# Kernel optimization log

Hardware: AMD Instinct MI355X
Metric: run time of the kernel (lower is better)

The kernel has to match this reference:

```python
import jax, jax.numpy as jnp
import numpy as np

D_MODEL = 1024
NUM_HEADS = 16
HEAD_DIM = D_MODEL // NUM_HEADS
B, T = 4, 2048


def setup_inputs() -> dict:
    key = jax.random.key(0)
    ks = jax.random.split(key, 6)
    s = 1.0 / np.sqrt(D_MODEL)  # ~ nn.Linear init scale
    return {
        "x_q": jax.random.normal(ks[0], (B, T, D_MODEL), jnp.float32),
        "x_kv": jax.random.normal(ks[1], (B, T, D_MODEL), jnp.float32),
        "Wq": jax.random.uniform(ks[2], (D_MODEL, D_MODEL), jnp.float32, -s, s),
        "Wk": jax.random.uniform(ks[3], (D_MODEL, D_MODEL), jnp.float32, -s, s),
        "Wv": jax.random.uniform(ks[4], (D_MODEL, D_MODEL), jnp.float32, -s, s),
        "Wo": jax.random.uniform(ks[5], (D_MODEL, D_MODEL), jnp.float32, -s, s),
    }


def reference(x_q, x_kv, Wq, Wk, Wv, Wo):
    Bq, Tq, C = x_q.shape
    Tk = x_kv.shape[1]
    # torch nn.Linear: y = x @ W.T
    q = (x_q @ Wq.T).reshape(Bq, Tq, NUM_HEADS, HEAD_DIM).transpose(0, 2, 1, 3)
    k = (x_kv @ Wk.T).reshape(Bq, Tk, NUM_HEADS, HEAD_DIM).transpose(0, 2, 1, 3)
    v = (x_kv @ Wv.T).reshape(Bq, Tk, NUM_HEADS, HEAD_DIM).transpose(0, 2, 1, 3)
    scores = jnp.einsum("bhqd,bhkd->bhqk", q, k) / jnp.sqrt(
        jnp.asarray(HEAD_DIM, x_q.dtype)
    )
    causal = jnp.triu(jnp.ones((Tq, Tk), bool), k=1)  # True above diagonal
    scores = jnp.where(causal, -jnp.inf, scores)
    attn = jax.nn.softmax(scores, axis=-1)
    out = jnp.einsum("bhqk,bhkd->bhqd", attn, v)
    out = out.transpose(0, 2, 1, 3).reshape(Bq, Tq, C)
    return out @ Wo.T
```

## Files before the change

### kernel.cpp

```cpp
#include <hip/hip_runtime.h>
#include <stdint.h>

#define T_SEQ 2048
#define NH 16
#define HD 64
#define DM 1024
#define BB 4
#define MROWS (BB * T_SEQ)

#define QSCALE 0.18033688011112042f

typedef __attribute__((ext_vector_type(8))) __bf16 bf16x8;
typedef __attribute__((ext_vector_type(8))) unsigned short u16x8;
typedef __attribute__((ext_vector_type(4))) unsigned short u16x4;
typedef __attribute__((ext_vector_type(4))) float f32x4;

__device__ __forceinline__ unsigned short f2bf(float f) {
  return __builtin_bit_cast(unsigned short, (__bf16)f);
}

__device__ __forceinline__ bf16x8 ld8_f32(const float* __restrict__ p) {
  f32x4 a = *(const f32x4*)p;
  f32x4 b = *(const f32x4*)(p + 4);
  u16x8 u;
#pragma unroll
  for (int i = 0; i < 4; ++i) {
    u[i]     = f2bf(a[i]);
    u[i + 4] = f2bf(b[i]);
  }
  return __builtin_bit_cast(bf16x8, u);
}

__device__ __forceinline__ bf16x8 ld8_bf(const unsigned short* p) {
  return __builtin_bit_cast(bf16x8, *(const u16x8*)p);
}

__device__ __forceinline__ bf16x8 ld8_lds(const unsigned short* p) {
  u16x4 a = *(const u16x4*)p;
  u16x4 b = *(const u16x4*)(p + 4);
  return __builtin_bit_cast(bf16x8,
      __builtin_shufflevector(a, b, 0, 1, 2, 3, 4, 5, 6, 7));
}

__device__ __forceinline__ u16x4 lo4(u16x8 v) {
  return __builtin_shufflevector(v, v, 0, 1, 2, 3);
}
__device__ __forceinline__ u16x4 hi4(u16x8 v) {
  return __builtin_shufflevector(v, v, 4, 5, 6, 7);
}

__device__ __forceinline__ void gload_lds16(const unsigned short* g,
                                            unsigned short* l) {
  __builtin_amdgcn_global_load_lds(
      (const __attribute__((address_space(1))) unsigned int*)g,
      (__attribute__((address_space(3))) unsigned int*)l, 16, 0, 0);
}

__global__ __launch_bounds__(256) void conv_stage1(
    const float* __restrict__ Wk, const float* __restrict__ Wv,
    const float* __restrict__ Wq, const float* __restrict__ Wo,
    const float* __restrict__ xkv, const float* __restrict__ xq,
    unsigned short* __restrict__ Wkb012, unsigned short* __restrict__ Wob,
    unsigned short* __restrict__ Sxkv, unsigned short* __restrict__ Sxq) {
  const int bid = blockIdx.x;
  const int WSEG = (DM * DM / 8) / 256;
  const int XSEG = (MROWS * DM / 8) / 256;
  if (bid < 4 * WSEG) {
    const int w = bid >> 9;
    const float* src = (w == 0) ? Wk : (w == 1) ? Wv : (w == 2) ? Wq : Wo;
    unsigned short* dst = (w < 3) ? Wkb012 + (size_t)w * DM * DM : Wob;
    const int i = (bid & (WSEG - 1)) * 256 + threadIdx.x;
    *(u16x8*)(dst + (size_t)i * 8) =
        __builtin_bit_cast(u16x8, ld8_f32(src + (size_t)i * 8));
  } else if (bid < 4 * WSEG + XSEG) {
    const int i = (bid - 4 * WSEG) * 256 + threadIdx.x;
    *(u16x8*)(Sxkv + (size_t)i * 8) =
        __builtin_bit_cast(u16x8, ld8_f32(xkv + (size_t)i * 8));
  } else {
    const int i = (bid - 4 * WSEG - XSEG) * 256 + threadIdx.x;
    *(u16x8*)(Sxq + (size_t)i * 8) =
        __builtin_bit_cast(u16x8, ld8_f32(xq + (size_t)i * 8));
  }
}

template <int MODE>
__global__ __launch_bounds__(256) void gemm128(
    const unsigned short* __restrict__ A, const unsigned short* __restrict__ A2,
    const unsigned short* __restrict__ B, void* __restrict__ Cv,
    void* __restrict__ Cv2, void* __restrict__ Cv3, int M, int N, int K) {
  __shared__ __align__(16) unsigned short As[2][2][128 * 32];
  __shared__ __align__(16) unsigned short Bs[2][2][128 * 32];

  const int t = threadIdx.x;
  const int lane = t & 63, wave = t >> 6;
  const int lin = (int)(blockIdx.x + gridDim.x * blockIdx.y);
  const int nx = N >> 7;
  const int mpx = (M >> 7) >> 3;
  const int xcd = lin & 7, slot = lin >> 3;
  const int m0 = (xcd * mpx + slot / nx) * 128;
  const int n0 = (slot % nx) * 128;

  const unsigned short* Ause = A;
  if constexpr (MODE == 5) {
    if (n0 >= 2 * DM) Ause = A2;
  }

  const int srow = t >> 2;
  const int scol = (t & 3) * 8;
  const unsigned short* ga0 = Ause + (size_t)(m0 + srow) * K + scol;
  const unsigned short* ga1 = Ause + (size_t)(m0 + 64 + srow) * K + scol;
  const unsigned short* gb0 = B + (size_t)(n0 + srow) * K + scol;
  const unsigned short* gb1 = B + (size_t)(n0 + 64 + srow) * K + scol;
  const int lo0 = (wave * 16) * 32, lo1 = (64 + wave * 16) * 32;

  const int mw = (wave >> 1) * 64, nw = (wave & 1) * 64;
  const int fr = lane & 15, fq = (lane >> 4) * 8;

  f32x4 acc[4][4];
#pragma unroll
  for (int i = 0; i < 4; ++i)
#pragma unroll
    for (int j = 0; j < 4; ++j) acc[i][j] = (f32x4){0.f, 0.f, 0.f, 0.f};

  auto stage = [&](int buf, int k0) {
    gload_lds16(ga0 + k0,      &As[buf][0][lo0]);
    gload_lds16(ga1 + k0,      &As[buf][0][lo1]);
    gload_lds16(gb0 + k0,      &Bs[buf][0][lo0]);
    gload_lds16(gb1 + k0,      &Bs[buf][0][lo1]);
    gload_lds16(ga0 + k0 + 32, &As[buf][1][lo0]);
    gload_lds16(ga1 + k0 + 32, &As[buf][1][lo1]);
    gload_lds16(gb0 + k0 + 32, &Bs[buf][1][lo0]);
    gload_lds16(gb1 + k0 + 32, &Bs[buf][1][lo1]);
  };

  stage(0, 0);
  __syncthreads();

  const int NT = K >> 6;
  int cur = 0;
  for (int kt = 0; kt < NT; ++kt) {
    if (kt + 1 < NT) stage(cur ^ 1, (kt + 1) << 6);
#pragma unroll
    for (int ks = 0; ks < 2; ++ks) {
      bf16x8 af[4], bfr[4];
#pragma unroll
      for (int i = 0; i < 4; ++i)
        af[i] = ld8_bf(&As[cur][ks][(mw + i * 16 + fr) * 32 + fq]);
#pragma unroll
      for (int j = 0; j < 4; ++j)
        bfr[j] = ld8_bf(&Bs[cur][ks][(nw + j * 16 + fr) * 32 + fq]);
#pragma unroll
      for (int i = 0; i < 4; ++i)
#pragma unroll
        for (int j = 0; j < 4; ++j)
          acc[i][j] = __builtin_amdgcn_mfma_f32_16x16x32_bf16(
              af[i], bfr[j], acc[i][j], 0, 0, 0);
    }
    __syncthreads();
    cur ^= 1;
  }

  const int orow = (lane >> 4) * 4, ocol = lane & 15;
#pragma unroll
  for (int i = 0; i < 4; ++i)
#pragma unroll
    for (int j = 0; j < 4; ++j) {
      const int mb = m0 + mw + i * 16 + orow;
      const int n = n0 + nw + j * 16 + ocol;
      if constexpr (MODE == 5) {
        if (n0 < DM) {
#pragma unroll
          for (int r = 0; r < 4; ++r)
            ((unsigned short*)Cv)[(size_t)(mb + r) * DM + n] =
                f2bf(acc[i][j][r]);
        } else if (n0 < 2 * DM) {
          const int nv = n - DM;
          u16x4 pk;
#pragma unroll
          for (int r = 0; r < 4; ++r) pk[r] = f2bf(acc[i][j][r]);
          unsigned short* dst = (unsigned short*)Cv2 +
              ((size_t)((mb >> 11) * NH + (nv >> 6)) * HD + (nv & 63)) *
                  T_SEQ +
              (mb & 2047);
          *(u16x4*)dst = pk;
        } else {
          const int nq = n - 2 * DM;
#pragma unroll
          for (int r = 0; r < 4; ++r)
            ((unsigned short*)Cv3)[(size_t)(mb + r) * DM + nq] =
                f2bf(acc[i][j][r] * QSCALE);
        }
      } else {
#pragma unroll
        for (int r = 0; r < 4; ++r)
          ((float*)Cv)[(size_t)(mb + r) * N + n] = acc[i][j][r];
      }
    }
}

#define ASTR 68

__global__ __launch_bounds__(256, 2) void attn_flash2(
    const unsigned short* Qw, const unsigned short* __restrict__ Kw,
    const unsigned short* __restrict__ Vt, unsigned short* Ow) {
  __shared__ __align__(16) unsigned short k_lds[2][64][ASTR];
  __shared__ __align__(16) unsigned short vt_lds[2][64][ASTR];
  __shared__ __align__(16) unsigned short p_lds[4][32][ASTR];

  const int tid = threadIdx.x, lane = tid & 63, wave = tid >> 6;
  const int c16 = lane & 15, quad = lane >> 4;
  const int b = blockIdx.z, h = blockIdx.y;
  const int pi = blockIdx.x;
  const int qb0A = (15 - pi) * 128;
  const int qb0B = pi * 128;
  const size_t rkbase = (size_t)b * T_SEQ * DM + (size_t)h * HD;
  const size_t vtbase = (size_t)(b * NH + h) * HD * T_SEQ;

  const int q_loA = qb0A + wave * 32;
  const int q_loB = qb0B + wave * 32;

  bf16x8 qfA[2][2], qfB[2][2];
#pragma unroll
  for (int nf = 0; nf < 2; ++nf) {
    const unsigned short* qpA =
        Qw + rkbase + (size_t)(q_loA + nf * 16 + c16) * DM + quad * 8;
    qfA[nf][0] = ld8_bf(qpA);
    qfA[nf][1] = ld8_bf(qpA + 32);
    const unsigned short* qpB =
        Qw + rkbase + (size_t)(q_loB + nf * 16 + c16) * DM + quad * 8;
    qfB[nf][0] = ld8_bf(qpB);
    qfB[nf][1] = ld8_bf(qpB + 32);
  }

  f32x4 oA[2][4], oB[2][4];
#pragma unroll
  for (int nf = 0; nf < 2; ++nf)
#pragma unroll
    for (int j = 0; j < 4; ++j) {
      oA[nf][j] = (f32x4){0.f, 0.f, 0.f, 0.f};
      oB[nf][j] = (f32x4){0.f, 0.f, 0.f, 0.f};
    }
  float mA[2] = {-3.0e38f, -3.0e38f}, lA[2] = {0.f, 0.f};
  float mB[2] = {-3.0e38f, -3.0e38f}, lB[2] = {0.f, 0.f};

  const int srow = tid >> 2;
  const int scol = (tid & 3) * 16;
  const int ntiles = (qb0A + 191) >> 6;
  const int ntA_w = (q_loA + 95) >> 6;
  const int ntB_w = (q_loB + 95) >> 6;

  const unsigned short* kp0 = Kw + rkbase + (size_t)srow * DM + scol;
  const unsigned short* vp0 = Vt + vtbase + (size_t)srow * T_SEQ + scol;

  auto subtile = [&](const bf16x8 (&qf)[2][2], f32x4 (&o)[2][4],
                     float (&m_r)[2], float (&l_r)[2], const int q_lo,
                     const int kb0, const int bi) {
    f32x4 s[4][2];
    __builtin_amdgcn_s_setprio(1);
#pragma unroll
    for (int mf = 0; mf < 4; ++mf) {
      const unsigned short* kr = &k_lds[bi][mf * 16 + c16][quad * 8];
      const bf16x8 k0 = ld8_lds(kr);
      const bf16x8 k1 = ld8_lds(kr + 32);
#pragma unroll
      for (int nf = 0; nf < 2; ++nf) {
        f32x4 a = {0.f, 0.f, 0.f, 0.f};
        a = __builtin_amdgcn_mfma_f32_16x16x32_bf16(k0, qf[nf][0], a, 0, 0, 0);
        a = __builtin_amdgcn_mfma_f32_16x16x32_bf16(k1, qf[nf][1], a, 0, 0, 0);
        s[mf][nf] = a;
      }
    }
    __builtin_amdgcn_s_setprio(0);
    if (kb0 + 63 > q_lo) {
#pragma unroll
      for (int mf = 0; mf < 4; ++mf) {
        const int key0 = kb0 + mf * 16 + quad * 4;
#pragma unroll
        for (int nf = 0; nf < 2; ++nf) {
          const int qg = q_lo + nf * 16 + c16;
#pragma unroll
          for (int r = 0; r < 4; ++r)
            if (key0 + r > qg) s[mf][nf][r] = -3.0e38f;
        }
      }
    }

#pragma unroll
    for (int nf = 0; nf < 2; ++nf) {
      float mx = -3.0e38f;
#pragma unroll
      for (int mf = 0; mf < 4; ++mf)
#pragma unroll
        for (int r = 0; r < 4; ++r) mx = fmaxf(mx, s[mf][nf][r]);
      mx = fmaxf(mx, __shfl_xor(mx, 16, 64));
      mx = fmaxf(mx, __shfl_xor(mx, 32, 64));
      if (!__all(mx - m_r[nf] <= 8.0f)) {
        const float m_new = fmaxf(m_r[nf], mx);
        const float al = exp2f(m_r[nf] - m_new);
        m_r[nf] = m_new;
        l_r[nf] *= al;
        float alr[4];
#pragma unroll
        for (int r = 0; r < 4; ++r) alr[r] = __shfl(al, quad * 4 + r, 16);
#pragma unroll
        for (int j = 0; j < 4; ++j)
#pragma unroll
          for (int r = 0; r < 4; ++r) o[nf][j][r] *= alr[r];
      }
      float ps = 0.f;
#pragma unroll
      for (int mf = 0; mf < 4; ++mf) {
        u16x4 pk;
#pragma unroll
        for (int r = 0; r < 4; ++r) {
          const float e = exp2f(s[mf][nf][r] - m_r[nf]);
          ps += e;
          pk[r] = f2bf(e);
        }
        *(u16x4*)&p_lds[wave][nf * 16 + c16][mf * 16 + quad * 4] = pk;
      }
      ps += __shfl_xor(ps, 16, 64);
      ps += __shfl_xor(ps, 32, 64);
      l_r[nf] += ps;
    }
    __threadfence_block();

    bf16x8 pf[2][2];
#pragma unroll
    for (int nf = 0; nf < 2; ++nf) {
      const unsigned short* pw = &p_lds[wave][nf * 16 + c16][quad * 8];
      pf[nf][0] = ld8_lds(pw);
      pf[nf][1] = ld8_lds(pw + 32);
    }
    __builtin_amdgcn_s_setprio(1);
#pragma unroll
    for (int j = 0; j < 4; ++j) {
      const unsigned short* vr = &vt_lds[bi][j * 16 + c16][quad * 8];
      const bf16x8 v0 = ld8_lds(vr);
      const bf16x8 v1 = ld8_lds(vr + 32);
#pragma unroll
      for (int nf = 0; nf < 2; ++nf) {
        o[nf][j] = __builtin_amdgcn_mfma_f32_16x16x32_bf16(pf[nf][0], v0,
                                                           o[nf][j], 0, 0, 0);
        o[nf][j] = __builtin_amdgcn_mfma_f32_16x16x32_bf16(pf[nf][1], v1,
                                                           o[nf][j], 0, 0, 0);
      }
    }
    __builtin_amdgcn_s_setprio(0);
  };

  {
    u16x8 ka = *(const u16x8*)kp0;
    u16x8 kc = *(const u16x8*)(kp0 + 8);
    u16x8 va = *(const u16x8*)vp0;
    u16x8 vc = *(const u16x8*)(vp0 + 8);
    *(u16x4*)&k_lds[0][srow][scol]       = lo4(ka);
    *(u16x4*)&k_lds[0][srow][scol + 4]   = hi4(ka);
    *(u16x4*)&k_lds[0][srow][scol + 8]   = lo4(kc);
    *(u16x4*)&k_lds[0][srow][scol + 12]  = hi4(kc);
    *(u16x4*)&vt_lds[0][srow][scol]      = lo4(va);
    *(u16x4*)&vt_lds[0][srow][scol + 4]  = hi4(va);
    *(u16x4*)&vt_lds[0][srow][scol + 8]  = lo4(vc);
    *(u16x4*)&vt_lds[0][srow][scol + 12] = hi4(vc);
  }
  __syncthreads();

  int cur = 0;
  for (int t = 0; t < ntiles; ++t) {
    const int kb0 = t * 64;
    const bool pf = (t + 1 < ntiles);
    u16x8 ka, kc, va, vc;
    if (pf) {
      const unsigned short* kp = kp0 + (size_t)(kb0 + 64) * DM;
      ka = *(const u16x8*)kp;
      kc = *(const u16x8*)(kp + 8);
      const unsigned short* vp = vp0 + (kb0 + 64);
      va = *(const u16x8*)vp;
      vc = *(const u16x8*)(vp + 8);
    }
    if (t < ntA_w) subtile(qfA, oA, mA, lA, q_loA, kb0, cur);
    if (t < ntB_w) subtile(qfB, oB, mB, lB, q_loB, kb0, cur);
    if (pf) {
      const int nb = cur ^ 1;
      *(u16x4*)&k_lds[nb][srow][scol]       = lo4(ka);
      *(u16x4*)&k_lds[nb][srow][scol + 4]   = hi4(ka);
      *(u16x4*)&k_lds[nb][srow][scol + 8]   = lo4(kc);
      *(u16x4*)&k_lds[nb][srow][scol + 12]  = hi4(kc);
      *(u16x4*)&vt_lds[nb][srow][scol]      = lo4(va);
      *(u16x4*)&vt_lds[nb][srow][scol + 4]  = hi4(va);
      *(u16x4*)&vt_lds[nb][srow][scol + 8]  = lo4(vc);
      *(u16x4*)&vt_lds[nb][srow][scol + 12] = hi4(vc);
      __syncthreads();
      cur = nb;
    }
  }

  auto epi = [&](f32x4 (&o)[2][4], float (&l_r)[2], const int q_lo) {
#pragma unroll
    for (int nf = 0; nf < 2; ++nf)
#pragma unroll
      for (int r = 0; r < 4; ++r) {
        const int qg = q_lo + nf * 16 + quad * 4 + r;
        const float inv = 1.0f / __shfl(l_r[nf], quad * 4 + r, 16);
        unsigned short* orow = Ow + rkbase + (size_t)qg * DM;
#pragma unroll
        for (int j = 0; j < 4; ++j)
          orow[j * 16 + c16] = f2bf(o[nf][j][r] * inv);
      }
  };
  epi(oA, lA, q_loA);
  epi(oB, lB, q_loB);
}

extern "C" void kernel_launch(void* const* d_in, const int* in_sizes, int n_in,
                              void* d_out, int out_size, void* d_ws, size_t ws_size,
                              hipStream_t stream) {
  const float* x_q  = (const float*)d_in[0];
  const float* x_kv = (const float*)d_in[1];
  const float* Wq   = (const float*)d_in[2];
  const float* Wk   = (const float*)d_in[3];
  const float* Wv   = (const float*)d_in[4];
  const float* Wo   = (const float*)d_in[5];
  float* out = (float*)d_out;

  unsigned short* Sxkv = (unsigned short*)d_out;
  unsigned short* Sxq  = Sxkv + (size_t)MROWS * DM;

  unsigned short* qb   = (unsigned short*)d_ws;
  unsigned short* kb   = qb + (size_t)MROWS * DM;
  unsigned short* vtb  = kb + (size_t)MROWS * DM;
  unsigned short* Wk_b = vtb + (size_t)MROWS * DM;
  unsigned short* Wo_b = Wk_b + (size_t)3 * DM * DM;

  const int nW8 = DM * DM / 8;
  const int nX8 = MROWS * DM / 8;

  conv_stage1<<<4 * (nW8 / 256) + 2 * (nX8 / 256), 256, 0, stream>>>(
      Wk, Wv, Wq, Wo, x_kv, x_q, Wk_b, Wo_b, Sxkv, Sxq);

  gemm128<5><<<dim3(3 * DM / 128, MROWS / 128), 256, 0, stream>>>(
      Sxkv, Sxq, Wk_b, kb, vtb, qb, MROWS, 3 * DM, DM);
  attn_flash2<<<dim3(8, NH, BB), 256, 0, stream>>>(qb, kb, vtb, qb);
  gemm128<1><<<dim3(DM / 128, MROWS / 128), 256, 0, stream>>>(
      qb, nullptr, Wo_b, out, nullptr, nullptr, MROWS, DM, DM);
}
```

Measured before the change: 287.7 us.

## Replace QKV projection GEMM with 256x256-tile, 512-thread swizzled-LDS kernel

The fused QKV projection moves from the 128x128-tile, 256-thread GEMM to a dedicated kernel with 256x256 output tiles, 8 waves, K-step 64 and XOR-swizzled LDS layout. Each wave computes a 128x64 sub-tile, and loads are double-buffered with explicit vmcnt waits, intra-iteration barriers and s_setprio around the MFMA bursts. The larger tiles raise arithmetic intensity and cut global traffic per FLOP, and the swizzle is meant to avoid LDS bank conflicts. In exchange the kernel needs more registers (128 accumulators per lane) and launches a smaller grid (384 blocks), which can leave some compute units idle or unevenly loaded.

```diff
diff --git a/kernel.cpp b/kernel.cpp
--- a/kernel.cpp
+++ b/kernel.cpp
@@ -83,11 +83,139 @@
   }
 }
 
+__global__ __launch_bounds__(512, 2) void gemm_qkv_p4(
+    const unsigned short* __restrict__ Axkv,
+    const unsigned short* __restrict__ Axq,
+    const unsigned short* __restrict__ B, unsigned short* __restrict__ Ck,
+    unsigned short* __restrict__ Cvt, unsigned short* __restrict__ Cq,
+    int M, int N, int K) {
+  __shared__ __align__(16) unsigned short As[2][2][128 * 64];
+  __shared__ __align__(16) unsigned short Bs[2][2][128 * 64];
+
+  const int t = threadIdx.x;
+  const int lane = t & 63, wave = t >> 6;
+  const int lin = (int)(blockIdx.x + gridDim.x * blockIdx.y);
+  const int nx = N >> 8;
+  const int mpx = (M >> 8) >> 3;
+  const int xcd = lin & 7, slot = lin >> 3;
+  const int m0 = (xcd * mpx + slot / nx) * 256;
+  const int n0 = (slot % nx) * 256;
+
+  const unsigned short* A = (n0 >= 2 * DM) ? Axq : Axkv;
+
+  const int tr = t >> 3;
+  const int tc = ((t & 7) ^ (tr & 7)) * 8;
+  const unsigned short* ga = A + (size_t)(m0 + tr) * K + tc;
+  const unsigned short* gb = B + (size_t)(n0 + tr) * K + tc;
+  const int ldst = wave * 512;
+
+  const int wm = wave >> 2, wn = wave & 3;
+  const int fr = lane & 15, quad = lane >> 4;
+  const int sw = fr & 7;
+
+  f32x4 acc[8][4];
+#pragma unroll
+  for (int i = 0; i < 8; ++i)
+#pragma unroll
+    for (int j = 0; j < 4; ++j) acc[i][j] = (f32x4){0.f, 0.f, 0.f, 0.f};
+
+  auto stage_tile = [&](int b, int k0) {
+#pragma unroll
+    for (int h = 0; h < 2; ++h)
+#pragma unroll
+      for (int c = 0; c < 2; ++c) {
+        gload_lds16(ga + (size_t)(h * 128 + c * 64) * K + k0,
+                    &As[b][h][c * 4096 + ldst]);
+        gload_lds16(gb + (size_t)(h * 128 + c * 64) * K + k0,
+                    &Bs[b][h][c * 4096 + ldst]);
+      }
+  };
+
+  stage_tile(0, 0);
+  stage_tile(1, 64);
+  asm volatile("s_waitcnt vmcnt(8)" ::: "memory");
+  __builtin_amdgcn_s_barrier();
+
+  const int NT = K >> 6;
+  for (int kt = 0; kt < NT; ++kt) {
+    const int cur = kt & 1;
+    bf16x8 bfr[2][4];
+#pragma unroll
+    for (int ks = 0; ks < 2; ++ks)
+#pragma unroll
+      for (int j = 0; j < 4; ++j) {
+        const int br = (wn & 1) * 64 + j * 16 + fr;
+        bfr[ks][j] =
+            ld8_bf(&Bs[cur][wn >> 1][br * 64 + ((ks * 4 + quad) ^ sw) * 8]);
+      }
+#pragma unroll
+    for (int p = 0; p < 4; ++p) {
+      bf16x8 af[2][2];
+#pragma unroll
+      for (int di = 0; di < 2; ++di)
+#pragma unroll
+        for (int ks = 0; ks < 2; ++ks) {
+          const int ar = (p * 2 + di) * 16 + fr;
+          af[di][ks] =
+              ld8_bf(&As[cur][wm][ar * 64 + ((ks * 4 + quad) ^ sw) * 8]);
+        }
+      __builtin_amdgcn_s_setprio(1);
+#pragma unroll
+      for (int di = 0; di < 2; ++di)
+#pragma unroll
+        for (int j = 0; j < 4; ++j)
+#pragma unroll
+          for (int ks = 0; ks < 2; ++ks)
+            acc[p * 2 + di][j] = __builtin_amdgcn_mfma_f32_16x16x32_bf16(
+                af[di][ks], bfr[ks][j], acc[p * 2 + di][j], 0, 0, 0);
+      __builtin_amdgcn_s_setprio(0);
+      if (p < 3) __builtin_amdgcn_s_barrier();
+    }
+    asm volatile("s_waitcnt lgkmcnt(0)" ::: "memory");
+    __builtin_amdgcn_s_barrier();
+    if (kt + 2 < NT) {
+      stage_tile(cur, (kt + 2) << 6);
+      asm volatile("s_waitcnt vmcnt(8)" ::: "memory");
+    } else {
+      asm volatile("s_waitcnt vmcnt(0)" ::: "memory");
+    }
+    __builtin_amdgcn_s_barrier();
+  }
+
+  const int orow = (lane >> 4) * 4, ocol = lane & 15;
+  const int mwo = wm * 128, nwo = wn * 64;
+#pragma unroll
+  for (int i = 0; i < 8; ++i)
+#pragma unroll
+    for (int j = 0; j < 4; ++j) {
+      const int mb = m0 + mwo + i * 16 + orow;
+      const int n = n0 + nwo + j * 16 + ocol;
+      if (n0 < DM) {
+#pragma unroll
+        for (int r = 0; r < 4; ++r)
+          Ck[(size_t)(mb + r) * DM + n] = f2bf(acc[i][j][r]);
+      } else if (n0 < 2 * DM) {
+        const int nv = n - DM;
+        u16x4 pk;
+#pragma unroll
+        for (int r = 0; r < 4; ++r) pk[r] = f2bf(acc[i][j][r]);
+        unsigned short* dst = Cvt +
+            ((size_t)((mb >> 11) * NH + (nv >> 6)) * HD + (nv & 63)) * T_SEQ +
+            (mb & 2047);
+        *(u16x4*)dst = pk;
+      } else {
+        const int nq = n - 2 * DM;
+#pragma unroll
+        for (int r = 0; r < 4; ++r)
+          Cq[(size_t)(mb + r) * DM + nq] = f2bf(acc[i][j][r] * QSCALE);
+      }
+    }
+}
+
 template <int MODE>
 __global__ __launch_bounds__(256) void gemm128(
-    const unsigned short* __restrict__ A, const unsigned short* __restrict__ A2,
-    const unsigned short* __restrict__ B, void* __restrict__ Cv,
-    void* __restrict__ Cv2, void* __restrict__ Cv3, int M, int N, int K) {
+    const unsigned short* __restrict__ A, const unsigned short* __restrict__ B,
+    void* __restrict__ Cv, int M, int N, int K) {
   __shared__ __align__(16) unsigned short As[2][2][128 * 32];
   __shared__ __align__(16) unsigned short Bs[2][2][128 * 32];
 
@@ -100,15 +228,10 @@
   const int m0 = (xcd * mpx + slot / nx) * 128;
   const int n0 = (slot % nx) * 128;
 
-  const unsigned short* Ause = A;
-  if constexpr (MODE == 5) {
-    if (n0 >= 2 * DM) Ause = A2;
-  }
-
   const int srow = t >> 2;
   const int scol = (t & 3) * 8;
-  const unsigned short* ga0 = Ause + (size_t)(m0 + srow) * K + scol;
-  const unsigned short* ga1 = Ause + (size_t)(m0 + 64 + srow) * K + scol;
+  const unsigned short* ga0 = A + (size_t)(m0 + srow) * K + scol;
+  const unsigned short* ga1 = A + (size_t)(m0 + 64 + srow) * K + scol;
   const unsigned short* gb0 = B + (size_t)(n0 + srow) * K + scol;
   const unsigned short* gb1 = B + (size_t)(n0 + 64 + srow) * K + scol;
   const int lo0 = (wave * 16) * 32, lo1 = (64 + wave * 16) * 32;
@@ -167,34 +290,9 @@
     for (int j = 0; j < 4; ++j) {
       const int mb = m0 + mw + i * 16 + orow;
       const int n = n0 + nw + j * 16 + ocol;
-      if constexpr (MODE == 5) {
-        if (n0 < DM) {
-#pragma unroll
-          for (int r = 0; r < 4; ++r)
-            ((unsigned short*)Cv)[(size_t)(mb + r) * DM + n] =
-                f2bf(acc[i][j][r]);
-        } else if (n0 < 2 * DM) {
-          const int nv = n - DM;
-          u16x4 pk;
-#pragma unroll
-          for (int r = 0; r < 4; ++r) pk[r] = f2bf(acc[i][j][r]);
-          unsigned short* dst = (unsigned short*)Cv2 +
-              ((size_t)((mb >> 11) * NH + (nv >> 6)) * HD + (nv & 63)) *
-                  T_SEQ +
-              (mb & 2047);
-          *(u16x4*)dst = pk;
-        } else {
-          const int nq = n - 2 * DM;
-#pragma unroll
-          for (int r = 0; r < 4; ++r)
-            ((unsigned short*)Cv3)[(size_t)(mb + r) * DM + nq] =
-                f2bf(acc[i][j][r] * QSCALE);
-        }
-      } else {
-#pragma unroll
-        for (int r = 0; r < 4; ++r)
-          ((float*)Cv)[(size_t)(mb + r) * N + n] = acc[i][j][r];
-      }
+#pragma unroll
+      for (int r = 0; r < 4; ++r)
+        ((float*)Cv)[(size_t)(mb + r) * N + n] = acc[i][j][r];
     }
 }
 
@@ -438,9 +536,9 @@
   conv_stage1<<<4 * (nW8 / 256) + 2 * (nX8 / 256), 256, 0, stream>>>(
       Wk, Wv, Wq, Wo, x_kv, x_q, Wk_b, Wo_b, Sxkv, Sxq);
 
-  gemm128<5><<<dim3(3 * DM / 128, MROWS / 128), 256, 0, stream>>>(
+  gemm_qkv_p4<<<dim3(3 * DM / 256, MROWS / 256), 512, 0, stream>>>(
       Sxkv, Sxq, Wk_b, kb, vtb, qb, MROWS, 3 * DM, DM);
   attn_flash2<<<dim3(8, NH, BB), 256, 0, stream>>>(qb, kb, vtb, qb);
   gemm128<1><<<dim3(DM / 128, MROWS / 128), 256, 0, stream>>>(
-      qb, nullptr, Wo_b, out, nullptr, nullptr, MROWS, DM, DM);
-}
+      qb, Wo_b, out, MROWS, DM, DM);
+}
```

New measurement: 299.6 us. 4.2% more time.

## Replace 128x128 GEMM with 512-thread 256-row tiled kernel using swizzled LDS

Applied to the files above, without the earlier changes.

Replaces the 256-thread 128x128 GEMM with a 512-thread kernel using 256-row tiles (256 or 128 columns) and 64-wide K steps. The LDS layout is XOR-swizzled to avoid bank conflicts. Loads are prefetched two tiles ahead with explicit vmcnt waits and raw barriers, and MFMA phases are wrapped in s_setprio. The fused QKV projection is split into one K/V launch and a separate Q launch. The aim is more data reuse per tile and better overlap of loads with compute, at the cost of more LDS, more registers and an extra kernel launch.

```diff
diff --git a/kernel.cpp b/kernel.cpp
--- a/kernel.cpp
+++ b/kernel.cpp
@@ -83,117 +83,149 @@
   }
 }
 
-template <int MODE>
-__global__ __launch_bounds__(256) void gemm128(
-    const unsigned short* __restrict__ A, const unsigned short* __restrict__ A2,
-    const unsigned short* __restrict__ B, void* __restrict__ Cv,
-    void* __restrict__ Cv2, void* __restrict__ Cv3, int M, int N, int K) {
-  __shared__ __align__(16) unsigned short As[2][2][128 * 32];
-  __shared__ __align__(16) unsigned short Bs[2][2][128 * 32];
+template <int BN, int MODE>
+__global__ __launch_bounds__(512, 2) void gemm_p4(
+    const unsigned short* __restrict__ A, const unsigned short* __restrict__ B,
+    void* __restrict__ C1, void* __restrict__ C2, int M, int N, int K) {
+  constexpr int BM = 256;
+  constexpr int BHALF = BN / 128;
+  constexpr int WM = (BN == 256) ? 2 : 4;
+  constexpr int RM = (BM / WM) / 16;
+  constexpr int PH = RM / 2;
+
+  __shared__ __align__(16) unsigned short As[2][2][128 * 64];
+  __shared__ __align__(16) unsigned short Bs[2][BHALF][128 * 64];
 
   const int t = threadIdx.x;
   const int lane = t & 63, wave = t >> 6;
   const int lin = (int)(blockIdx.x + gridDim.x * blockIdx.y);
-  const int nx = N >> 7;
-  const int mpx = (M >> 7) >> 3;
+  const int nx = N / BN;
+  const int mpx = (M >> 8) >> 3;
   const int xcd = lin & 7, slot = lin >> 3;
-  const int m0 = (xcd * mpx + slot / nx) * 128;
-  const int n0 = (slot % nx) * 128;
-
-  const unsigned short* Ause = A;
-  if constexpr (MODE == 5) {
-    if (n0 >= 2 * DM) Ause = A2;
-  }
-
-  const int srow = t >> 2;
-  const int scol = (t & 3) * 8;
-  const unsigned short* ga0 = Ause + (size_t)(m0 + srow) * K + scol;
-  const unsigned short* ga1 = Ause + (size_t)(m0 + 64 + srow) * K + scol;
-  const unsigned short* gb0 = B + (size_t)(n0 + srow) * K + scol;
-  const unsigned short* gb1 = B + (size_t)(n0 + 64 + srow) * K + scol;
-  const int lo0 = (wave * 16) * 32, lo1 = (64 + wave * 16) * 32;
-
-  const int mw = (wave >> 1) * 64, nw = (wave & 1) * 64;
-  const int fr = lane & 15, fq = (lane >> 4) * 8;
-
-  f32x4 acc[4][4];
-#pragma unroll
-  for (int i = 0; i < 4; ++i)
+  const int m0 = (xcd * mpx + slot / nx) * BM;
+  const int n0 = (slot % nx) * BN;
+
+  const int tr = t >> 3;
+  const int tc = ((t & 7) ^ (tr & 7)) * 8;
+  const unsigned short* ga = A + (size_t)(m0 + tr) * K + tc;
+  const unsigned short* gb = B + (size_t)(n0 + tr) * K + tc;
+  const int ldst = wave * 512;
+
+  const int wm = (BN == 256) ? (wave >> 2) : (wave >> 1);
+  const int wn = (BN == 256) ? (wave & 3) : (wave & 1);
+  const int fr = lane & 15, quad = lane >> 4;
+  const int sw = fr & 7;
+
+  f32x4 acc[RM][4];
+#pragma unroll
+  for (int i = 0; i < RM; ++i)
 #pragma unroll
     for (int j = 0; j < 4; ++j) acc[i][j] = (f32x4){0.f, 0.f, 0.f, 0.f};
 
-  auto stage = [&](int buf, int k0) {
-    gload_lds16(ga0 + k0,      &As[buf][0][lo0]);
-    gload_lds16(ga1 + k0,      &As[buf][0][lo1]);
-    gload_lds16(gb0 + k0,      &Bs[buf][0][lo0]);
-    gload_lds16(gb1 + k0,      &Bs[buf][0][lo1]);
-    gload_lds16(ga0 + k0 + 32, &As[buf][1][lo0]);
-    gload_lds16(ga1 + k0 + 32, &As[buf][1][lo1]);
-    gload_lds16(gb0 + k0 + 32, &Bs[buf][1][lo0]);
-    gload_lds16(gb1 + k0 + 32, &Bs[buf][1][lo1]);
+  auto stage_tile = [&](int b, int k0) {
+#pragma unroll
+    for (int h = 0; h < 4; ++h)
+      gload_lds16(ga + (size_t)(h * 64) * K + k0,
+                  &As[b][h >> 1][(h & 1) * 4096 + ldst]);
+#pragma unroll
+    for (int h = 0; h < 2 * BHALF; ++h)
+      gload_lds16(gb + (size_t)(h * 64) * K + k0,
+                  &Bs[b][h >> 1][(h & 1) * 4096 + ldst]);
   };
 
-  stage(0, 0);
-  __syncthreads();
+  stage_tile(0, 0);
+  stage_tile(1, 64);
+  if constexpr (BN == 256)
+    asm volatile("s_waitcnt vmcnt(8)" ::: "memory");
+  else
+    asm volatile("s_waitcnt vmcnt(6)" ::: "memory");
+  __builtin_amdgcn_s_barrier();
 
   const int NT = K >> 6;
-  int cur = 0;
   for (int kt = 0; kt < NT; ++kt) {
-    if (kt + 1 < NT) stage(cur ^ 1, (kt + 1) << 6);
-#pragma unroll
-    for (int ks = 0; ks < 2; ++ks) {
-      bf16x8 af[4], bfr[4];
-#pragma unroll
-      for (int i = 0; i < 4; ++i)
-        af[i] = ld8_bf(&As[cur][ks][(mw + i * 16 + fr) * 32 + fq]);
-#pragma unroll
-      for (int j = 0; j < 4; ++j)
-        bfr[j] = ld8_bf(&Bs[cur][ks][(nw + j * 16 + fr) * 32 + fq]);
-#pragma unroll
-      for (int i = 0; i < 4; ++i)
+    const int cur = kt & 1;
+    bf16x8 bfr[2][4];
+    const int bh = (BN == 256) ? (wn >> 1) : 0;
+    const int brb = (BN == 256) ? (wn & 1) * 64 : wn * 64;
+#pragma unroll
+    for (int ks = 0; ks < 2; ++ks)
+#pragma unroll
+      for (int j = 0; j < 4; ++j) {
+        const int br = brb + j * 16 + fr;
+        bfr[ks][j] =
+            ld8_bf(&Bs[cur][bh][br * 64 + ((ks * 4 + quad) ^ sw) * 8]);
+      }
+#pragma unroll
+    for (int p = 0; p < PH; ++p) {
+      bf16x8 af[2][2];
+#pragma unroll
+      for (int di = 0; di < 2; ++di)
+#pragma unroll
+        for (int ks = 0; ks < 2; ++ks) {
+          const int ar = wm * (BM / WM) + (p * 2 + di) * 16 + fr;
+          af[di][ks] = ld8_bf(
+              &As[cur][ar >> 7][(ar & 127) * 64 + ((ks * 4 + quad) ^ sw) * 8]);
+        }
+      __builtin_amdgcn_s_setprio(1);
+#pragma unroll
+      for (int di = 0; di < 2; ++di)
 #pragma unroll
         for (int j = 0; j < 4; ++j)
-          acc[i][j] = __builtin_amdgcn_mfma_f32_16x16x32_bf16(
-              af[i], bfr[j], acc[i][j], 0, 0, 0);
-    }
-    __syncthreads();
-    cur ^= 1;
+#pragma unroll
+          for (int ks = 0; ks < 2; ++ks)
+            acc[p * 2 + di][j] = __builtin_amdgcn_mfma_f32_16x16x32_bf16(
+                af[di][ks], bfr[ks][j], acc[p * 2 + di][j], 0, 0, 0);
+      __builtin_amdgcn_s_setprio(0);
+      if (p < PH - 1) __builtin_amdgcn_s_barrier();
+    }
+    asm volatile("s_waitcnt lgkmcnt(0)" ::: "memory");
+    __builtin_amdgcn_s_barrier();
+    if (kt + 2 < NT) {
+      stage_tile(cur, (kt + 2) << 6);
+      if constexpr (BN == 256)
+        asm volatile("s_waitcnt vmcnt(8)" ::: "memory");
+      else
+        asm volatile("s_waitcnt vmcnt(6)" ::: "memory");
+    } else {
+      asm volatile("s_waitcnt vmcnt(0)" ::: "memory");
+    }
+    __builtin_amdgcn_s_barrier();
   }
 
   const int orow = (lane >> 4) * 4, ocol = lane & 15;
-#pragma unroll
-  for (int i = 0; i < 4; ++i)
+  const int mwo = wm * (BM / WM), nwo = wn * 64;
+#pragma unroll
+  for (int i = 0; i < RM; ++i)
 #pragma unroll
     for (int j = 0; j < 4; ++j) {
-      const int mb = m0 + mw + i * 16 + orow;
-      const int n = n0 + nw + j * 16 + ocol;
-      if constexpr (MODE == 5) {
+      const int mb = m0 + mwo + i * 16 + orow;
+      const int n = n0 + nwo + j * 16 + ocol;
+      if constexpr (MODE == 3) {
         if (n0 < DM) {
 #pragma unroll
           for (int r = 0; r < 4; ++r)
-            ((unsigned short*)Cv)[(size_t)(mb + r) * DM + n] =
+            ((unsigned short*)C1)[(size_t)(mb + r) * DM + n] =
                 f2bf(acc[i][j][r]);
-        } else if (n0 < 2 * DM) {
+        } else {
           const int nv = n - DM;
           u16x4 pk;
 #pragma unroll
           for (int r = 0; r < 4; ++r) pk[r] = f2bf(acc[i][j][r]);
-          unsigned short* dst = (unsigned short*)Cv2 +
+          unsigned short* dst = (unsigned short*)C2 +
               ((size_t)((mb >> 11) * NH + (nv >> 6)) * HD + (nv & 63)) *
                   T_SEQ +
               (mb & 2047);
           *(u16x4*)dst = pk;
-        } else {
-          const int nq = n - 2 * DM;
-#pragma unroll
-          for (int r = 0; r < 4; ++r)
-            ((unsigned short*)Cv3)[(size_t)(mb + r) * DM + nq] =
-                f2bf(acc[i][j][r] * QSCALE);
         }
+      } else if constexpr (MODE == 4) {
+#pragma unroll
+        for (int r = 0; r < 4; ++r)
+          ((unsigned short*)C1)[(size_t)(mb + r) * N + n] =
+              f2bf(acc[i][j][r] * QSCALE);
       } else {
 #pragma unroll
         for (int r = 0; r < 4; ++r)
-          ((float*)Cv)[(size_t)(mb + r) * N + n] = acc[i][j][r];
+          ((float*)C1)[(size_t)(mb + r) * N + n] = acc[i][j][r];
       }
     }
 }
@@ -430,6 +462,7 @@
   unsigned short* kb   = qb + (size_t)MROWS * DM;
   unsigned short* vtb  = kb + (size_t)MROWS * DM;
   unsigned short* Wk_b = vtb + (size_t)MROWS * DM;
+  unsigned short* Wq_b = Wk_b + (size_t)2 * DM * DM;
   unsigned short* Wo_b = Wk_b + (size_t)3 * DM * DM;
 
   const int nW8 = DM * DM / 8;
@@ -438,9 +471,11 @@
   conv_stage1<<<4 * (nW8 / 256) + 2 * (nX8 / 256), 256, 0, stream>>>(
       Wk, Wv, Wq, Wo, x_kv, x_q, Wk_b, Wo_b, Sxkv, Sxq);
 
-  gemm128<5><<<dim3(3 * DM / 128, MROWS / 128), 256, 0, stream>>>(
-      Sxkv, Sxq, Wk_b, kb, vtb, qb, MROWS, 3 * DM, DM);
+  gemm_p4<256, 3><<<dim3(2 * DM / 256, MROWS / 256), 512, 0, stream>>>(
+      Sxkv, Wk_b, kb, vtb, MROWS, 2 * DM, DM);
+  gemm_p4<128, 4><<<dim3(DM / 128, MROWS / 256), 512, 0, stream>>>(
+      Sxq, Wq_b, qb, nullptr, MROWS, DM, DM);
   attn_flash2<<<dim3(8, NH, BB), 256, 0, stream>>>(qb, kb, vtb, qb);
-  gemm128<1><<<dim3(DM / 128, MROWS / 128), 256, 0, stream>>>(
-      qb, nullptr, Wo_b, out, nullptr, nullptr, MROWS, DM, DM);
-}
+  gemm_p4<128, 1><<<dim3(DM / 128, MROWS / 256), 512, 0, stream>>>(
+      qb, Wo_b, out, nullptr, MROWS, DM, DM);
+}
```

After: 294.2 us. 2.3% more time.
